# Optimization experiments

Measured on AMD Instinct MI355X. Metric: run time of the kernel, lower is better.

## Reference

```python
import jax, jax.numpy as jnp
import numpy as np

B, L, C, H = 2, 4096, 512, 8
DH = C // H


def setup_inputs() -> dict:
    key = jax.random.key(0)
    ks = jax.random.split(key, 6)
    s = 1.0 / np.sqrt(C)
    return {
        "x": jax.random.normal(ks[0], (B, L, C), dtype=jnp.float32),
        "Wq": jax.random.normal(ks[1], (C, C), dtype=jnp.float32) * s,
        "Wk": jax.random.normal(ks[2], (C, C), dtype=jnp.float32) * s,
        "Wv": jax.random.normal(ks[3], (C, C), dtype=jnp.float32) * s,
        "Wo": jax.random.normal(ks[4], (C, C), dtype=jnp.float32) * s,
        "bo": jnp.zeros((C,), dtype=jnp.float32),
    }


def reference(x, Wq, Wk, Wv, Wo, bo):
    # x: [B, L, C]; split heads -> [B, H, L, Dh]
    def heads(t):
        return t.reshape(B, L, H, DH).transpose(0, 2, 1, 3)

    q = heads(x @ Wq)
    k = heads(x @ Wk)
    v = heads(x @ Wv)
    scale = 1.0 / np.sqrt(DH)
    scores = jnp.einsum("bhqd,bhkd->bhqk", q, k) * scale  # [B,H,L,L]
    w = jax.nn.softmax(scores, axis=-1)  # dropout_rate=0.0 -> identity
    att = jnp.einsum("bhqk,bhkd->bhqd", w, v)  # [B,H,L,Dh]
    att = att.transpose(0, 2, 1, 3).reshape(B, L, C)
    return att @ Wo + bo
```

## Files before the change

### kernel.cpp

```cpp
#include <hip/hip_runtime.h>
#include <hip/hip_bf16.h>

typedef __hip_bfloat16 bh;
typedef __attribute__((ext_vector_type(8))) __bf16 bf16x8;
typedef __attribute__((ext_vector_type(4))) float f32x4;
typedef __attribute__((ext_vector_type(4))) int i32x4;
typedef __attribute__((ext_vector_type(4))) short s16x4;

#define NB 2
#define NL 4096
#define NC 512
#define NH 8
#define NDH 64
#define NM (NB * NL)
#define LOG2E 1.4426950408889634f
#define KVBLK 8192

static __device__ __forceinline__ f32x4 mfma_bf16(bf16x8 a, bf16x8 b, f32x4 c) {
    return __builtin_amdgcn_mfma_f32_16x16x32_bf16(a, b, c, 0, 0, 0);
}

static __device__ __forceinline__ void st_bf4(bh* dst, float a, float b, float c, float d) {
    bh tmp[4] = {__float2bfloat16(a), __float2bfloat16(b),
                 __float2bfloat16(c), __float2bfloat16(d)};
    *(s16x4*)dst = *(const s16x4*)tmp;
}
static __device__ __forceinline__ bf16x8 pk_bf8(float a0, float a1, float a2, float a3,
                                                float b0, float b1, float b2, float b3) {
    bh tmp[8] = {__float2bfloat16(a0), __float2bfloat16(a1),
                 __float2bfloat16(a2), __float2bfloat16(a3),
                 __float2bfloat16(b0), __float2bfloat16(b1),
                 __float2bfloat16(b2), __float2bfloat16(b3)};
    return *(const bf16x8*)tmp;
}

static __device__ __forceinline__ void gload16(const bh* g, bh* l) {
    __builtin_amdgcn_global_load_lds(
        (const __attribute__((address_space(1))) void*)g,
        (__attribute__((address_space(3))) void*)l,
        16, 0, 0);
}

__global__ __launch_bounds__(256, 2)
void prep(const float* __restrict__ x,
          const float* __restrict__ Wq, const float* __restrict__ Wk,
          const float* __restrict__ Wv, const float* __restrict__ Wo,
          bh* __restrict__ xf, bh* __restrict__ Wf)
{
    const int t = threadIdx.x;
    const int wave = t >> 6, lane = t & 63;
    const int quad = lane >> 4, c16 = lane & 15;

    if (blockIdx.z < 8) {
        __shared__ __align__(16) bh T[64][72];
        const int m64 = blockIdx.x, k64 = blockIdx.z;
        #pragma unroll
        for (int rep = 0; rep < 4; rep++) {
            int li = t + rep * 256;
            int r = li >> 4, c4 = (li & 15) * 4;
            float4 f = *(const float4*)&x[(size_t)(m64 * 64 + r) * 512 + k64 * 64 + c4];
            st_bf4(&T[r][c4], f.x, f.y, f.z, f.w);
        }
        __syncthreads();
        #pragma unroll
        for (int kcl = 0; kcl < 2; kcl++) {
            i32x4 v = *(const i32x4*)&T[wave * 16 + c16][kcl * 32 + quad * 8];
            size_t addr = ((size_t)(m64 * 4 + wave) * 16 + (k64 * 2 + kcl)) * 512 + lane * 8;
            *(i32x4*)&xf[addr] = v;
        }
    } else {
        if (blockIdx.x >= 64) return;
        int task = blockIdx.x * 4 + wave;
        int z = task >> 6, nt = (task >> 3) & 7, k0i = task & 7;
        const float* W = (z == 0) ? Wq : (z == 1) ? Wk : (z == 2) ? Wv : Wo;
        bh* dst = Wf + (((size_t)z * 8 + nt) * 8 + k0i) * 4096;
        #pragma unroll
        for (int kc = 0; kc < 2; kc++)
            #pragma unroll
            for (int fn = 0; fn < 4; fn++) {
                bh tmp[8];
                #pragma unroll
                for (int j = 0; j < 8; j++)
                    tmp[j] = __float2bfloat16(
                        W[(size_t)(k0i * 64 + kc * 32 + quad * 8 + j) * 512
                          + nt * 64 + fn * 16 + c16]);
                *(i32x4*)&dst[(kc * 4 + fn) * 512 + lane * 8] = *(const i32x4*)tmp;
            }
    }
}

__global__ __launch_bounds__(256, 4)
void qkv_gemm(const bh* __restrict__ xf, const bh* __restrict__ Wf,
              bh* __restrict__ Qb, bh* __restrict__ KVf)
{
    __shared__ __align__(16) bh smem[2][8192];

    const int t = threadIdx.x;
    const int wave = t >> 6, lane = t & 63;
    const int quad = lane >> 4, c16 = lane & 15;
    const int m0 = blockIdx.x * 64;
    const int nt = blockIdx.y;
    const int m16b = m0 >> 4;

    f32x4 acc[3][4];
    for (int z = 0; z < 3; z++)
        for (int fn = 0; fn < 4; fn++)
            for (int u = 0; u < 4; u++) acc[z][fn][u] = 0.0f;

    auto stage = [&](int k32, int buf) {
        bh* Xl = &smem[buf][0];
        bh* Wl = &smem[buf][2048];
        gload16(xf + ((size_t)(m16b + wave) * 16 + k32) * 512 + lane * 8,
                &Xl[wave * 512 + lane * 8]);
        #pragma unroll
        for (int z = 0; z < 3; z++) {
            const bh* wz = Wf + (((size_t)z * 8 + nt) * 8 + (k32 >> 1)) * 4096
                         + (size_t)((k32 & 1) * 4 + wave) * 512;
            gload16(wz + lane * 8, &Wl[z * 2048 + wave * 512 + lane * 8]);
        }
    };

    stage(0, 0);
    for (int k32 = 0; k32 < 16; k32++) {
        const int buf = k32 & 1;
        __syncthreads();
        if (k32 < 15) stage(k32 + 1, buf ^ 1);
        const bh* Xl = &smem[buf][0];
        const bh* Wl = &smem[buf][2048];
        bf16x8 af = *(const bf16x8*)&Xl[wave * 512 + lane * 8];
        #pragma unroll
        for (int z = 0; z < 3; z++)
            #pragma unroll
            for (int fn = 0; fn < 4; fn++) {
                bf16x8 bf = *(const bf16x8*)&Wl[z * 2048 + fn * 512 + lane * 8];
                acc[z][fn] = mfma_bf16(af, bf, acc[z][fn]);
            }
    }
    __syncthreads();

    const int h = nt;
    const int b = m0 >> 12;
    const int l0 = m0 & 4095;
    const int bh_i = b * NH + h;
    const int kt0 = l0 >> 6;

    {
        bh* Tq = &smem[0][0];
        #pragma unroll
        for (int i = 0; i < 4; i++) {
            int ll = wave * 16 + quad * 4 + i;
            #pragma unroll
            for (int fn = 0; fn < 4; fn++)
                Tq[ll * 68 + fn * 16 + c16] =
                    __float2bfloat16(acc[0][fn][i] * 0.125f);
        }
        __syncthreads();
        int l = t >> 2, part = t & 3;
        bh* dst = Qb + ((size_t)bh_i * NL + l0 + l) * NDH + part * 16;
        const bh* src = &Tq[l * 68 + part * 16];
        *(i32x4*)(dst)     = *(const i32x4*)(src);
        *(i32x4*)(dst + 8) = *(const i32x4*)(src + 8);
        __syncthreads();
    }

    {
        bh* Tk = &smem[0][0];
        #pragma unroll
        for (int i = 0; i < 4; i++) {
            int c16t = quad * 4 + i;
            #pragma unroll
            for (int fn = 0; fn < 4; fn++) {
                int d = fn * 16 + c16;
                int kc = d >> 5, qt = (d >> 3) & 3, j = d & 7;
                Tk[(wave * 2 + kc) * 512 + (qt * 16 + c16t) * 8 + j] =
                    __float2bfloat16(acc[1][fn][i] * LOG2E);
            }
        }
        __syncthreads();
        int idx = t * 16;
        bh* dst = KVf + (size_t)(bh_i * 64 + kt0) * KVBLK + idx;
        *(i32x4*)(dst)     = *(const i32x4*)&Tk[idx];
        *(i32x4*)(dst + 8) = *(const i32x4*)&Tk[idx + 8];
    }

    #pragma unroll
    for (int fn = 0; fn < 4; fn++) {
        size_t addr = (size_t)(bh_i * 64 + kt0) * KVBLK + 4096
                    + (size_t)(fn * 2 + (wave >> 1)) * 512 + lane * 8 + (wave & 1) * 4;
        st_bf4(&KVf[addr], acc[2][fn][0], acc[2][fn][1],
                           acc[2][fn][2], acc[2][fn][3]);
    }
}

__global__ __launch_bounds__(512, 4)
void flash_attn(const bh* __restrict__ Qb, const bh* __restrict__ KVf,
                bh* __restrict__ attb)
{
    __shared__ __align__(16) bh SF[2][2][KVBLK];

    const int t = threadIdx.x;
    const int wave = t >> 6, lane = t & 63;
    const int group = wave >> 2, w4 = wave & 3;
    const int quad = lane >> 4, c16 = lane & 15;

    const int bid = blockIdx.x + blockIdx.y * 32;
    const int work = (bid & 7) * 64 + (bid >> 3);
    const int bh_idx = work >> 5;
    const int q0 = (work & 31) * 128;

    const bh* Qp  = Qb + (size_t)bh_idx * NL * NDH;
    const bh* KVp = KVf + (size_t)bh_idx * 64 * KVBLK;

    bf16x8 qf[2][2];
    #pragma unroll
    for (int fq = 0; fq < 2; fq++)
        #pragma unroll
        for (int kc = 0; kc < 2; kc++)
            qf[fq][kc] = *(const bf16x8*)
                &Qp[(size_t)(q0 + w4 * 32 + fq * 16 + c16) * NDH + kc * 32 + quad * 8];

    f32x4 ot[4][2];
    float lsum[2] = {0.0f, 0.0f};
    for (int a = 0; a < 4; a++)
        for (int fq = 0; fq < 2; fq++)
            for (int u = 0; u < 4; u++) ot[a][fq][u] = 0.0f;
    const f32x4 z4 = {0.0f, 0.0f, 0.0f, 0.0f};

    auto stage = [&](int i, int buf) {
        int kt = 2 * i + group;
        #pragma unroll
        for (int r = 0; r < 4; r++) {
            int off = (w4 * 4 + r) * 512 + lane * 8;
            gload16(KVp + (size_t)kt * KVBLK + off, &SF[group][buf][off]);
        }
    };

    stage(0, 0);
    for (int i = 0; i < 32; i++) {
        const int buf = i & 1;
        __syncthreads();
        if (i < 31) stage(i + 1, buf ^ 1);
        const bh* sf = &SF[group][buf][0];

        f32x4 s[4][2];
        #pragma unroll
        for (int fk = 0; fk < 4; fk++) {
            bf16x8 kf0 = *(const bf16x8*)&sf[(fk * 2 + 0) * 512 + lane * 8];
            s[fk][0] = mfma_bf16(kf0, qf[0][0], z4);
            s[fk][1] = mfma_bf16(kf0, qf[1][0], z4);
        }
        #pragma unroll
        for (int fk = 0; fk < 4; fk++) {
            bf16x8 kf1 = *(const bf16x8*)&sf[(fk * 2 + 1) * 512 + lane * 8];
            s[fk][0] = mfma_bf16(kf1, qf[0][1], s[fk][0]);
            s[fk][1] = mfma_bf16(kf1, qf[1][1], s[fk][1]);
        }

        bf16x8 vt[4][2];
        #pragma unroll
        for (int fn = 0; fn < 4; fn++)
            #pragma unroll
            for (int a = 0; a < 2; a++)
                vt[fn][a] = *(const bf16x8*)&sf[4096 + (fn * 2 + a) * 512 + lane * 8];

        float rs0 = 0.0f, rs1 = 0.0f;
        #pragma unroll
        for (int a = 0; a < 2; a++) {
            float a0 = __builtin_amdgcn_exp2f(s[2 * a][0][0]);
            float a1 = __builtin_amdgcn_exp2f(s[2 * a][0][1]);
            float a2 = __builtin_amdgcn_exp2f(s[2 * a][0][2]);
            float a3 = __builtin_amdgcn_exp2f(s[2 * a][0][3]);
            float a4 = __builtin_amdgcn_exp2f(s[2 * a + 1][0][0]);
            float a5 = __builtin_amdgcn_exp2f(s[2 * a + 1][0][1]);
            float a6 = __builtin_amdgcn_exp2f(s[2 * a + 1][0][2]);
            float a7 = __builtin_amdgcn_exp2f(s[2 * a + 1][0][3]);
            rs0 += ((a0 + a1) + (a2 + a3)) + ((a4 + a5) + (a6 + a7));
            bf16x8 p0 = pk_bf8(a0, a1, a2, a3, a4, a5, a6, a7);
            float b0 = __builtin_amdgcn_exp2f(s[2 * a][1][0]);
            float b1 = __builtin_amdgcn_exp2f(s[2 * a][1][1]);
            float b2 = __builtin_amdgcn_exp2f(s[2 * a][1][2]);
            float b3 = __builtin_amdgcn_exp2f(s[2 * a][1][3]);
            float b4 = __builtin_amdgcn_exp2f(s[2 * a + 1][1][0]);
            float b5 = __builtin_amdgcn_exp2f(s[2 * a + 1][1][1]);
            float b6 = __builtin_amdgcn_exp2f(s[2 * a + 1][1][2]);
            float b7 = __builtin_amdgcn_exp2f(s[2 * a + 1][1][3]);
            rs1 += ((b0 + b1) + (b2 + b3)) + ((b4 + b5) + (b6 + b7));
            bf16x8 p1 = pk_bf8(b0, b1, b2, b3, b4, b5, b6, b7);
            #pragma unroll
            for (int fn = 0; fn < 4; fn++) {
                ot[fn][0] = mfma_bf16(vt[fn][a], p0, ot[fn][0]);
                ot[fn][1] = mfma_bf16(vt[fn][a], p1, ot[fn][1]);
            }
        }
        lsum[0] += rs0;
        lsum[1] += rs1;
    }

    #pragma unroll
    for (int fq = 0; fq < 2; fq++) {
        lsum[fq] += __shfl_xor(lsum[fq], 16);
        lsum[fq] += __shfl_xor(lsum[fq], 32);
    }

    float* Ocmb = (float*)&SF[0][0][0];
    float* Lcmb = Ocmb + 128 * 64;
    __syncthreads();
    if (group == 1) {
        #pragma unroll
        for (int fq = 0; fq < 2; fq++) {
            int q = w4 * 32 + fq * 16 + c16;
            #pragma unroll
            for (int fn = 0; fn < 4; fn++)
                *(f32x4*)&Ocmb[q * 64 + fn * 16 + quad * 4] = ot[fn][fq];
            if (quad == 0) Lcmb[q] = lsum[fq];
        }
    }
    __syncthreads();
    if (group == 0) {
        const int b = bh_idx >> 3, h = bh_idx & 7;
        const int mbase16 = (b * NL + q0) >> 4;
        #pragma unroll
        for (int fq = 0; fq < 2; fq++) {
            int q = w4 * 32 + fq * 16 + c16;
            float inv = 1.0f / (lsum[fq] + Lcmb[q]);
            int m16 = mbase16 + w4 * 2 + fq;
            #pragma unroll
            for (int fn = 0; fn < 4; fn++) {
                f32x4 o2 = *(const f32x4*)&Ocmb[q * 64 + fn * 16 + quad * 4];
                size_t addr = ((size_t)m16 * 16 + h * 2 + (fn >> 1)) * 512
                            + (size_t)(((fn & 1) * 2 + (quad >> 1)) * 16 + c16) * 8
                            + (quad & 1) * 4;
                st_bf4(&attb[addr],
                       (ot[fn][fq][0] + o2[0]) * inv, (ot[fn][fq][1] + o2[1]) * inv,
                       (ot[fn][fq][2] + o2[2]) * inv, (ot[fn][fq][3] + o2[3]) * inv);
            }
        }
    }
}

__global__ __launch_bounds__(256, 4)
void out_gemm(const bh* __restrict__ Af, const bh* __restrict__ Wf,
              const float* __restrict__ bo, float* __restrict__ out)
{
    __shared__ __align__(16) bh smem[2][4096];

    const int t = threadIdx.x;
    const int wave = t >> 6, lane = t & 63;
    const int quad = lane >> 4, c16 = lane & 15;
    const int m0 = blockIdx.x * 64;
    const int nt = blockIdx.y;
    const int n0 = nt * 64;
    const int m16b = m0 >> 4;

    f32x4 acc[4];
    for (int fn = 0; fn < 4; fn++)
        for (int u = 0; u < 4; u++) acc[fn][u] = 0.0f;

    auto stage = [&](int k32, int buf) {
        bh* Xl = &smem[buf][0];
        bh* Wl = &smem[buf][2048];
        gload16(Af + ((size_t)(m16b + wave) * 16 + k32) * 512 + lane * 8,
                &Xl[wave * 512 + lane * 8]);
        const bh* wz = Wf + (((size_t)3 * 8 + nt) * 8 + (k32 >> 1)) * 4096
                     + (size_t)((k32 & 1) * 4 + wave) * 512;
        gload16(wz + lane * 8, &Wl[wave * 512 + lane * 8]);
    };

    stage(0, 0);
    for (int k32 = 0; k32 < 16; k32++) {
        const int buf = k32 & 1;
        __syncthreads();
        if (k32 < 15) stage(k32 + 1, buf ^ 1);
        const bh* Xl = &smem[buf][0];
        const bh* Wl = &smem[buf][2048];
        bf16x8 af = *(const bf16x8*)&Xl[wave * 512 + lane * 8];
        #pragma unroll
        for (int fn = 0; fn < 4; fn++) {
            bf16x8 bf = *(const bf16x8*)&Wl[fn * 512 + lane * 8];
            acc[fn] = mfma_bf16(af, bf, acc[fn]);
        }
    }

    #pragma unroll
    for (int i = 0; i < 4; i++) {
        int mr = m0 + wave * 16 + quad * 4 + i;
        #pragma unroll
        for (int fn = 0; fn < 4; fn++) {
            int cn = n0 + fn * 16 + c16;
            out[(size_t)mr * 512 + cn] = acc[fn][i] + bo[cn];
        }
    }
}

extern "C" void kernel_launch(void* const* d_in, const int* in_sizes, int n_in,
                              void* d_out, int out_size, void* d_ws, size_t ws_size,
                              hipStream_t stream)
{
    const float* x  = (const float*)d_in[0];
    const float* Wq = (const float*)d_in[1];
    const float* Wk = (const float*)d_in[2];
    const float* Wv = (const float*)d_in[3];
    const float* Wo = (const float*)d_in[4];
    const float* bo = (const float*)d_in[5];
    float* out = (float*)d_out;

    const size_t mat = (size_t)NM * NC;
    bh* Qb   = (bh*)d_ws;
    bh* KVf  = Qb + mat;
    bh* attb = KVf + 2 * mat;
    bh* Wf   = attb + mat;
    bh* xf   = Wf + 4 * 8 * 8 * 4096;

    prep      <<<dim3(128, 1, 9),         256, 0, stream>>>(x, Wq, Wk, Wv, Wo, xf, Wf);
    qkv_gemm  <<<dim3(NM / 64, NC / 64),  256, 0, stream>>>(xf, Wf, Qb, KVf);
    flash_attn<<<dim3(NL / 128, NB * NH), 512, 0, stream>>>(Qb, KVf, attb);
    out_gemm  <<<dim3(NM / 64, NC / 64),  256, 0, stream>>>(attb, Wf, bo, out);
}
```

Baseline: 178.6 us.

## Fuse x fp32-to-bf16 conversion into QKV GEMM and load A operands directly

Drops the x conversion pass from the prep kernel. The QKV GEMM now reads fp32 x straight from global memory into registers, converts it to a bf16 fragment in-kernel, and prefetches the next k-slice. The out GEMM likewise loads its A fragment directly into registers instead of staging it through LDS, which shrinks its shared memory. This removes an extra read and write of x and one pass of LDS traffic, but every column-tile block (8 per row tile) now re-reads fp32 x with partly uncoalesced per-lane row accesses.

Result: no change. 178.1 us (-0.3%).

```diff
diff --git a/kernel.cpp b/kernel.cpp
--- a/kernel.cpp
+++ b/kernel.cpp
@@ -42,76 +42,53 @@
 }
 
 __global__ __launch_bounds__(256, 2)
-void prep(const float* __restrict__ x,
-          const float* __restrict__ Wq, const float* __restrict__ Wk,
+void prep(const float* __restrict__ Wq, const float* __restrict__ Wk,
           const float* __restrict__ Wv, const float* __restrict__ Wo,
-          bh* __restrict__ xf, bh* __restrict__ Wf)
+          bh* __restrict__ Wf)
 {
     const int t = threadIdx.x;
     const int wave = t >> 6, lane = t & 63;
     const int quad = lane >> 4, c16 = lane & 15;
 
-    if (blockIdx.z < 8) {
-        __shared__ __align__(16) bh T[64][72];
-        const int m64 = blockIdx.x, k64 = blockIdx.z;
-        #pragma unroll
-        for (int rep = 0; rep < 4; rep++) {
-            int li = t + rep * 256;
-            int r = li >> 4, c4 = (li & 15) * 4;
-            float4 f = *(const float4*)&x[(size_t)(m64 * 64 + r) * 512 + k64 * 64 + c4];
-            st_bf4(&T[r][c4], f.x, f.y, f.z, f.w);
-        }
-        __syncthreads();
-        #pragma unroll
-        for (int kcl = 0; kcl < 2; kcl++) {
-            i32x4 v = *(const i32x4*)&T[wave * 16 + c16][kcl * 32 + quad * 8];
-            size_t addr = ((size_t)(m64 * 4 + wave) * 16 + (k64 * 2 + kcl)) * 512 + lane * 8;
-            *(i32x4*)&xf[addr] = v;
-        }
-    } else {
-        if (blockIdx.x >= 64) return;
-        int task = blockIdx.x * 4 + wave;
-        int z = task >> 6, nt = (task >> 3) & 7, k0i = task & 7;
-        const float* W = (z == 0) ? Wq : (z == 1) ? Wk : (z == 2) ? Wv : Wo;
-        bh* dst = Wf + (((size_t)z * 8 + nt) * 8 + k0i) * 4096;
-        #pragma unroll
-        for (int kc = 0; kc < 2; kc++)
-            #pragma unroll
-            for (int fn = 0; fn < 4; fn++) {
-                bh tmp[8];
-                #pragma unroll
-                for (int j = 0; j < 8; j++)
-                    tmp[j] = __float2bfloat16(
-                        W[(size_t)(k0i * 64 + kc * 32 + quad * 8 + j) * 512
-                          + nt * 64 + fn * 16 + c16]);
-                *(i32x4*)&dst[(kc * 4 + fn) * 512 + lane * 8] = *(const i32x4*)tmp;
-            }
-    }
+    int task = blockIdx.x * 4 + wave;
+    int z = task >> 6, nt = (task >> 3) & 7, k0i = task & 7;
+    const float* W = (z == 0) ? Wq : (z == 1) ? Wk : (z == 2) ? Wv : Wo;
+    bh* dst = Wf + (((size_t)z * 8 + nt) * 8 + k0i) * 4096;
+    #pragma unroll
+    for (int kc = 0; kc < 2; kc++)
+        #pragma unroll
+        for (int fn = 0; fn < 4; fn++) {
+            bh tmp[8];
+            #pragma unroll
+            for (int j = 0; j < 8; j++)
+                tmp[j] = __float2bfloat16(
+                    W[(size_t)(k0i * 64 + kc * 32 + quad * 8 + j) * 512
+                      + nt * 64 + fn * 16 + c16]);
+            *(i32x4*)&dst[(kc * 4 + fn) * 512 + lane * 8] = *(const i32x4*)tmp;
+        }
 }
 
 __global__ __launch_bounds__(256, 4)
-void qkv_gemm(const bh* __restrict__ xf, const bh* __restrict__ Wf,
+void qkv_gemm(const float* __restrict__ x, const bh* __restrict__ Wf,
               bh* __restrict__ Qb, bh* __restrict__ KVf)
 {
-    __shared__ __align__(16) bh smem[2][8192];
+    __shared__ __align__(16) bh smem[2][6144];
 
     const int t = threadIdx.x;
     const int wave = t >> 6, lane = t & 63;
     const int quad = lane >> 4, c16 = lane & 15;
     const int m0 = blockIdx.x * 64;
     const int nt = blockIdx.y;
-    const int m16b = m0 >> 4;
+
+    const float* xrow = x + (size_t)(m0 + wave * 16 + c16) * 512 + quad * 8;
 
     f32x4 acc[3][4];
     for (int z = 0; z < 3; z++)
         for (int fn = 0; fn < 4; fn++)
             for (int u = 0; u < 4; u++) acc[z][fn][u] = 0.0f;
 
-    auto stage = [&](int k32, int buf) {
-        bh* Xl = &smem[buf][0];
-        bh* Wl = &smem[buf][2048];
-        gload16(xf + ((size_t)(m16b + wave) * 16 + k32) * 512 + lane * 8,
-                &Xl[wave * 512 + lane * 8]);
+    auto stageW = [&](int k32, int buf) {
+        bh* Wl = &smem[buf][0];
         #pragma unroll
         for (int z = 0; z < 3; z++) {
             const bh* wz = Wf + (((size_t)z * 8 + nt) * 8 + (k32 >> 1)) * 4096
@@ -120,14 +97,19 @@
         }
     };
 
-    stage(0, 0);
+    float4 ax0 = *(const float4*)&xrow[0];
+    float4 ax1 = *(const float4*)&xrow[4];
+    stageW(0, 0);
     for (int k32 = 0; k32 < 16; k32++) {
         const int buf = k32 & 1;
         __syncthreads();
-        if (k32 < 15) stage(k32 + 1, buf ^ 1);
-        const bh* Xl = &smem[buf][0];
-        const bh* Wl = &smem[buf][2048];
-        bf16x8 af = *(const bf16x8*)&Xl[wave * 512 + lane * 8];
+        if (k32 < 15) stageW(k32 + 1, buf ^ 1);
+        const int kn = (k32 < 15) ? (k32 + 1) * 32 : 15 * 32;
+        float4 nx0 = *(const float4*)&xrow[kn];
+        float4 nx1 = *(const float4*)&xrow[kn + 4];
+        bf16x8 af = pk_bf8(ax0.x, ax0.y, ax0.z, ax0.w,
+                           ax1.x, ax1.y, ax1.z, ax1.w);
+        const bh* Wl = &smem[buf][0];
         #pragma unroll
         for (int z = 0; z < 3; z++)
             #pragma unroll
@@ -135,6 +117,7 @@
                 bf16x8 bf = *(const bf16x8*)&Wl[z * 2048 + fn * 512 + lane * 8];
                 acc[z][fn] = mfma_bf16(af, bf, acc[z][fn]);
             }
+        ax0 = nx0; ax1 = nx1;
     }
     __syncthreads();
 
@@ -342,7 +325,7 @@
 void out_gemm(const bh* __restrict__ Af, const bh* __restrict__ Wf,
               const float* __restrict__ bo, float* __restrict__ out)
 {
-    __shared__ __align__(16) bh smem[2][4096];
+    __shared__ __align__(16) bh smem[2][2048];
 
     const int t = threadIdx.x;
     const int wave = t >> 6, lane = t & 63;
@@ -352,33 +335,34 @@
     const int n0 = nt * 64;
     const int m16b = m0 >> 4;
 
+    const bh* arow = Af + ((size_t)(m16b + wave) * 16) * 512 + lane * 8;
+
     f32x4 acc[4];
     for (int fn = 0; fn < 4; fn++)
         for (int u = 0; u < 4; u++) acc[fn][u] = 0.0f;
 
-    auto stage = [&](int k32, int buf) {
-        bh* Xl = &smem[buf][0];
-        bh* Wl = &smem[buf][2048];
-        gload16(Af + ((size_t)(m16b + wave) * 16 + k32) * 512 + lane * 8,
-                &Xl[wave * 512 + lane * 8]);
+    auto stageW = [&](int k32, int buf) {
         const bh* wz = Wf + (((size_t)3 * 8 + nt) * 8 + (k32 >> 1)) * 4096
                      + (size_t)((k32 & 1) * 4 + wave) * 512;
-        gload16(wz + lane * 8, &Wl[wave * 512 + lane * 8]);
+        gload16(wz + lane * 8, &smem[buf][wave * 512 + lane * 8]);
     };
 
-    stage(0, 0);
+    i32x4 axc = *(const i32x4*)&arow[0];
+    stageW(0, 0);
     for (int k32 = 0; k32 < 16; k32++) {
         const int buf = k32 & 1;
         __syncthreads();
-        if (k32 < 15) stage(k32 + 1, buf ^ 1);
-        const bh* Xl = &smem[buf][0];
-        const bh* Wl = &smem[buf][2048];
-        bf16x8 af = *(const bf16x8*)&Xl[wave * 512 + lane * 8];
+        if (k32 < 15) stageW(k32 + 1, buf ^ 1);
+        const int kn = (k32 < 15) ? (k32 + 1) : 15;
+        i32x4 axn = *(const i32x4*)&arow[(size_t)kn * 512];
+        bf16x8 af = *(const bf16x8*)&axc;
+        const bh* Wl = &smem[buf][0];
         #pragma unroll
         for (int fn = 0; fn < 4; fn++) {
             bf16x8 bf = *(const bf16x8*)&Wl[fn * 512 + lane * 8];
             acc[fn] = mfma_bf16(af, bf, acc[fn]);
         }
+        axc = axn;
     }
 
     #pragma unroll
@@ -409,10 +393,9 @@
     bh* KVf  = Qb + mat;
     bh* attb = KVf + 2 * mat;
     bh* Wf   = attb + mat;
-    bh* xf   = Wf + 4 * 8 * 8 * 4096;
-
-    prep      <<<dim3(128, 1, 9),         256, 0, stream>>>(x, Wq, Wk, Wv, Wo, xf, Wf);
-    qkv_gemm  <<<dim3(NM / 64, NC / 64),  256, 0, stream>>>(xf, Wf, Qb, KVf);
+
+    prep      <<<dim3(64, 1, 1),          256, 0, stream>>>(Wq, Wk, Wv, Wo, Wf);
+    qkv_gemm  <<<dim3(NM / 64, NC / 64),  256, 0, stream>>>(x, Wf, Qb, KVf);
     flash_attn<<<dim3(NL / 128, NB * NH), 512, 0, stream>>>(Qb, KVf, attb);
     out_gemm  <<<dim3(NM / 64, NC / 64),  256, 0, stream>>>(attb, Wf, bo, out);
 }
```
